# Kernel optimization log

Hardware: AMD Instinct MI355X
Metric: run time of the kernel (lower is better)

The kernel has to match this reference:

```python
import jax, jax.numpy as jnp
import numpy as np

B, T, E, D, A, V, EMB = 256, 64, 2048, 512, 512, 10000, 256

def _glorot(key, shape):
    lim = np.sqrt(6.0 / (shape[0] + shape[-1]))
    return jax.random.uniform(key, shape, jnp.float32, -lim, lim)

def setup_inputs() -> dict:
    key = jax.random.key(0)
    ks = jax.random.split(key, 16)
    return {
        'input_c': jax.random.randint(ks[0], (B, 1), 0, V),
        'hidden': jax.random.normal(ks[1], (B, D), jnp.float32),
        'carry': jax.random.normal(ks[2], (B, D), jnp.float32),
        'encoder_output': jax.random.normal(ks[3], (B, T, E), jnp.float32),
        'emb': jax.random.normal(ks[4], (V, EMB), jnp.float32) * 0.05,
        'w1': _glorot(ks[5], (D, A)),  'b1': jnp.zeros((A,), jnp.float32),
        'w2': _glorot(ks[6], (E, A)),  'b2': jnp.zeros((A,), jnp.float32),
        'v':  _glorot(ks[7], (A, 1)),  'bv': jnp.zeros((1,), jnp.float32),
        'wx': _glorot(ks[8], (E + EMB, 4 * D)),
        'wh': _glorot(ks[9], (D, 4 * D)),
        'bl': jnp.zeros((4 * D,), jnp.float32),
        'wp': _glorot(ks[10], (D, V)), 'bp': jnp.zeros((V,), jnp.float32),
    }

def reference(input_c, hidden, carry, encoder_output, emb, w1, b1, w2, b2, v, bv, wx, wh, bl, wp, bp):
    # embedding: [B,1] -> [B,EMB] after squeeze
    x = emb[input_c[:, 0]]
    # Bahdanau additive attention: score = v^T tanh(W1 h + W2 enc)
    q = hidden @ w1 + b1                                # [B,A]
    k = jnp.einsum('bte,ea->bta', encoder_output, w2) + b2  # [B,T,A]
    score = jnp.tanh(q[:, None, :] + k) @ v + bv        # [B,T,1]
    attn = jax.nn.softmax(score, axis=1)                # [B,T,1]
    context = jnp.sum(attn * encoder_output, axis=1)    # [B,E]
    # LSTM cell (keras gate order i,f,c,o); dropout inactive (training=False)
    lstm_in = jnp.concatenate([context, x], axis=-1)    # [B,E+EMB]
    z = lstm_in @ wx + hidden @ wh + bl                 # [B,4D]
    i, f, g, o = jnp.split(z, 4, axis=-1)
    c_new = jax.nn.sigmoid(f) * carry + jax.nn.sigmoid(i) * jnp.tanh(g)
    h_new = jax.nn.sigmoid(o) * jnp.tanh(c_new)
    logits = h_new @ wp + bp                            # [B,V]
    return logits, h_new, c_new
```

## Files before the change

### kernel.cpp

```cpp
#include <hip/hip_runtime.h>
#include <hip/hip_bf16.h>
#include <math.h>

#define BB 256
#define TT 64
#define EE 2048
#define DD 512
#define AA 512
#define VV 10000
#define VPAD 10240
#define EMBD 256
#define KLSTM (EE + EMBD + DD)
#define N4D (4 * DD)
#define MROWS (BB * TT)

using bf16x8 = __attribute__((ext_vector_type(8))) __bf16;
using f32x4  = __attribute__((ext_vector_type(4))) float;

#define GLL16(gp, lp) __builtin_amdgcn_global_load_lds( \
    (const __attribute__((address_space(1))) void*)(gp), \
    (__attribute__((address_space(3))) void*)(lp), 16, 0, 0)

__device__ __forceinline__ float sigf(float x) { return 1.f / (1.f + expf(-x)); }

__global__ void k_wt(const float* __restrict__ w2, const float* __restrict__ wx,
                     const float* __restrict__ wh, const float* __restrict__ wp,
                     __bf16* __restrict__ w2t, __bf16* __restrict__ wxh_t,
                     __bf16* __restrict__ wpt) {
    __shared__ float t[32][33];
    const int bid = blockIdx.x;
    const int tid = threadIdx.x;
    const int tx = tid & 31, ty = tid >> 5;

    if (bid < 1024) {
        const int k0 = (bid & 63) * 32, n0 = (bid >> 6) * 32;
        #pragma unroll
        for (int i = 0; i < 4; ++i)
            t[ty + 8 * i][tx] = w2[(size_t)(k0 + ty + 8 * i) * AA + n0 + tx];
        __syncthreads();
        #pragma unroll
        for (int i = 0; i < 4; ++i)
            w2t[(size_t)(n0 + ty + 8 * i) * EE + k0 + tx] = (__bf16)t[tx][ty + 8 * i];
    } else if (bid < 6656) {
        const int idx = bid - 1024;
        const int k0 = (idx % 88) * 32, n0 = (idx / 88) * 32;
        #pragma unroll
        for (int i = 0; i < 4; ++i) {
            int k = k0 + ty + 8 * i;
            const float* wrow = (k < EE + EMBD) ? &wx[(size_t)k * N4D]
                                                : &wh[(size_t)(k - EE - EMBD) * N4D];
            t[ty + 8 * i][tx] = wrow[n0 + tx];
        }
        __syncthreads();
        #pragma unroll
        for (int i = 0; i < 4; ++i)
            wxh_t[(size_t)(n0 + ty + 8 * i) * KLSTM + k0 + tx] = (__bf16)t[tx][ty + 8 * i];
    } else {
        const int idx = bid - 6656;
        const int k0 = (idx & 15) * 32, n0 = (idx >> 4) * 32;
        #pragma unroll
        for (int i = 0; i < 4; ++i) {
            int n = n0 + tx;
            t[ty + 8 * i][tx] = wp[(size_t)(k0 + ty + 8 * i) * VV + (n < VV ? n : VV - 1)];
        }
        __syncthreads();
        #pragma unroll
        for (int i = 0; i < 4; ++i)
            wpt[(size_t)(n0 + ty + 8 * i) * DD + k0 + tx] = (__bf16)t[tx][ty + 8 * i];
    }
}

__global__ void k_q(const float* __restrict__ hidden, const float* __restrict__ w1,
                    const float* __restrict__ b1, const float* __restrict__ b2,
                    float* __restrict__ qq) {
    __shared__ float hs[DD];
    const int b = blockIdx.x, tid = threadIdx.x;
    {
        float2 hv = *(const float2*)&hidden[(size_t)b * DD + 2 * tid];
        hs[2 * tid] = hv.x; hs[2 * tid + 1] = hv.y;
    }
    __syncthreads();
    const int a0 = 2 * tid;
    float2 acc = {0.f, 0.f};
    #pragma unroll 4
    for (int k = 0; k < DD; ++k) {
        float2 w = *(const float2*)&w1[(size_t)k * AA + a0];
        float h = hs[k];
        acc.x = fmaf(h, w.x, acc.x);
        acc.y = fmaf(h, w.y, acc.y);
    }
    qq[(size_t)b * AA + a0]     = acc.x + b1[a0]     + b2[a0];
    qq[(size_t)b * AA + a0 + 1] = acc.y + b1[a0 + 1] + b2[a0 + 1];
}

__global__ __launch_bounds__(1024, 8) void k_score(
        const float* __restrict__ enc, const __bf16* __restrict__ w2t,
        const float* __restrict__ qq, const float* __restrict__ vvec,
        float* __restrict__ spart) {
    __shared__ bf16x8 Abuf[128][8];
    __shared__ bf16x8 Bbuf[128][8];
    __shared__ float vsv[128];
    __shared__ float qsv2[2][128];
    __shared__ float wredL[16][32];
    const int tid = threadIdx.x;
    const int mb = blockIdx.x & 127, nb = blockIdx.x >> 7;
    const int m0 = mb * 128, n0 = nb * 128;
    const int l = tid & 63, wv = tid >> 6;
    const int wm = wv >> 2, wn = wv & 3;
    const int ar = l & 15, agr = l >> 4;

    if (tid < 256) {
        int i = tid >> 7, col = tid & 127;
        qsv2[i][col] = qq[(size_t)(2 * mb + i) * AA + n0 + col];
    } else if (tid < 384) {
        vsv[tid - 256] = vvec[n0 + tid - 256];
    }

    const int arow = tid >> 3, ag = tid & 7;
    const float* aptr = enc + (size_t)(m0 + arow) * EE + ag * 8;

    const int brow0 = wv * 8;
    const __bf16* bsrc = w2t + (size_t)(n0 + brow0 + (l >> 3)) * EE
                             + ((l & 7) ^ (l >> 3)) * 8;

    f32x4 acc[2][2];
    #pragma unroll
    for (int mi = 0; mi < 2; ++mi)
        #pragma unroll
        for (int ni = 0; ni < 2; ++ni)
            acc[mi][ni] = (f32x4){0.f, 0.f, 0.f, 0.f};

    const int NIT = EE / 64;
    for (int it = 0; it < NIT; ++it) {
        if (it > 0) __syncthreads();
        GLL16(bsrc + it * 64, &Bbuf[brow0][0]);
        {
            float4 u0 = *(const float4*)(aptr + it * 64);
            float4 u1 = *(const float4*)(aptr + it * 64 + 4);
            bf16x8 pk;
            pk[0] = (__bf16)u0.x; pk[1] = (__bf16)u0.y; pk[2] = (__bf16)u0.z; pk[3] = (__bf16)u0.w;
            pk[4] = (__bf16)u1.x; pk[5] = (__bf16)u1.y; pk[6] = (__bf16)u1.z; pk[7] = (__bf16)u1.w;
            Abuf[arow][ag ^ (arow & 7)] = pk;
        }
        __syncthreads();
        #pragma unroll
        for (int ks = 0; ks < 2; ++ks) {
            bf16x8 afr[2], bfr[2];
            #pragma unroll
            for (int mi = 0; mi < 2; ++mi)
                afr[mi] = Abuf[wm * 32 + mi * 16 + ar][(ks * 4 + agr) ^ (ar & 7)];
            #pragma unroll
            for (int ni = 0; ni < 2; ++ni)
                bfr[ni] = Bbuf[wn * 32 + ni * 16 + ar][(ks * 4 + agr) ^ (ar & 7)];
            #pragma unroll
            for (int mi = 0; mi < 2; ++mi)
                #pragma unroll
                for (int ni = 0; ni < 2; ++ni)
                    acc[mi][ni] = __builtin_amdgcn_mfma_f32_16x16x32_bf16(afr[mi], bfr[ni], acc[mi][ni], 0, 0, 0);
        }
    }

    float sred[2][4];
    #pragma unroll
    for (int mi = 0; mi < 2; ++mi)
        #pragma unroll
        for (int r = 0; r < 4; ++r) sred[mi][r] = 0.f;
    #pragma unroll
    for (int ni = 0; ni < 2; ++ni) {
        const int col = wn * 32 + ni * 16 + ar;
        const float va = vsv[col];
        const float qa = qsv2[wm >> 1][col];
        #pragma unroll
        for (int mi = 0; mi < 2; ++mi)
            #pragma unroll
            for (int r = 0; r < 4; ++r)
                sred[mi][r] += tanhf(qa + acc[mi][ni][r]) * va;
    }
    #pragma unroll
    for (int mi = 0; mi < 2; ++mi)
        #pragma unroll
        for (int r = 0; r < 4; ++r) {
            #pragma unroll
            for (int off = 1; off < 16; off <<= 1)
                sred[mi][r] += __shfl_xor(sred[mi][r], off, 64);
        }
    if (ar == 0) {
        #pragma unroll
        for (int mi = 0; mi < 2; ++mi)
            #pragma unroll
            for (int r = 0; r < 4; ++r)
                wredL[wv][mi * 16 + agr * 4 + r] = sred[mi][r];
    }
    __syncthreads();
    if (tid < 128) {
        const int wm4 = tid >> 5, rloc = tid & 31;
        float s = wredL[wm4 * 4 + 0][rloc] + wredL[wm4 * 4 + 1][rloc]
                + wredL[wm4 * 4 + 2][rloc] + wredL[wm4 * 4 + 3][rloc];
        spart[(size_t)nb * MROWS + m0 + tid] = s;
    }
}

__global__ void k_context(const float* __restrict__ enc, const float* __restrict__ spart,
                          const float* __restrict__ bv, float* __restrict__ ctx) {
    __shared__ float attn[TT];
    const int b = blockIdx.y;
    const int tid = threadIdx.x;
    if (tid < 64) {
        const int m = b * TT + tid;
        float s = spart[m] + spart[MROWS + m] + spart[2 * MROWS + m] + spart[3 * MROWS + m] + bv[0];
        float mx = s;
        #pragma unroll
        for (int off = 1; off < 64; off <<= 1) mx = fmaxf(mx, __shfl_xor(mx, off, 64));
        float p = expf(s - mx);
        float sum = p;
        #pragma unroll
        for (int off = 1; off < 64; off <<= 1) sum += __shfl_xor(sum, off, 64);
        attn[tid] = p / sum;
    }
    __syncthreads();
    const int e = blockIdx.x * 1024 + tid * 4;
    const float* encb = enc + (size_t)b * TT * EE + e;
    float4 acc = {0.f, 0.f, 0.f, 0.f};
    #pragma unroll 4
    for (int t = 0; t < TT; ++t) {
        float a = attn[t];
        float4 ev = *(const float4*)&encb[(size_t)t * EE];
        acc.x = fmaf(a, ev.x, acc.x);
        acc.y = fmaf(a, ev.y, acc.y);
        acc.z = fmaf(a, ev.z, acc.z);
        acc.w = fmaf(a, ev.w, acc.w);
    }
    *(float4*)&ctx[(size_t)b * EE + e] = acc;
}

#define ZKS 4
#define ZKC (KLSTM / ZKS)
#define ZNIT (ZKC / 32)
__global__ void k_z(const float* __restrict__ ctx, const float* __restrict__ emb,
                    const int* __restrict__ cidx, const float* __restrict__ hidden,
                    const __bf16* __restrict__ wt, float* __restrict__ zp) {
    __shared__ bf16x8 Abuf[32][ZKC / 8];
    __shared__ int cbs[32];
    const int tid = threadIdx.x;
    const int l = tid & 63, wv = tid >> 6;
    const int b0  = blockIdx.y * 32;
    const int kc0 = blockIdx.z * ZKC;
    const int nw  = blockIdx.x * 256 + wv * 64;

    if (tid < 32) cbs[tid] = cidx[b0 + tid];
    __syncthreads();

    {
        const int srow = tid >> 3, g0 = tid & 7;
        const int bg = b0 + srow;
        const int erow = cbs[srow];
        #pragma unroll
        for (int i = 0; i < 11; ++i) {
            int g = g0 + 8 * i;
            int k = kc0 + g * 8;
            const float* src;
            if (k < EE)             src = &ctx[(size_t)bg * EE + k];
            else if (k < EE + EMBD) src = &emb[(size_t)erow * EMBD + (k - EE)];
            else                    src = &hidden[(size_t)bg * DD + (k - EE - EMBD)];
            float4 u0 = *(const float4*)src;
            float4 u1 = *(const float4*)(src + 4);
            bf16x8 pk;
            pk[0] = (__bf16)u0.x; pk[1] = (__bf16)u0.y; pk[2] = (__bf16)u0.z; pk[3] = (__bf16)u0.w;
            pk[4] = (__bf16)u1.x; pk[5] = (__bf16)u1.y; pk[6] = (__bf16)u1.z; pk[7] = (__bf16)u1.w;
            Abuf[srow][g ^ (srow & 7)] = pk;
        }
    }
    __syncthreads();

    const int ar = l & 15, agr = l >> 4;
    const __bf16* bbase = wt + (size_t)(nw + ar) * KLSTM + kc0 + agr * 8;

    f32x4 acc[2][4];
    #pragma unroll
    for (int mt = 0; mt < 2; ++mt)
        #pragma unroll
        for (int f = 0; f < 4; ++f)
            acc[mt][f] = (f32x4){0.f, 0.f, 0.f, 0.f};

    bf16x8 bA[4], bBv[4];
    #pragma unroll
    for (int f = 0; f < 4; ++f)
        bA[f] = *(const bf16x8*)(bbase + (size_t)f * 16 * KLSTM);

    for (int itp = 0; itp < ZNIT / 2; ++itp) {
        const int it0 = 2 * itp, it1 = 2 * itp + 1;
        #pragma unroll
        for (int f = 0; f < 4; ++f)
            bBv[f] = *(const bf16x8*)(bbase + (size_t)f * 16 * KLSTM + it1 * 32);
        {
            bf16x8 a0 = Abuf[ar][(it0 * 4 + agr) ^ (ar & 7)];
            bf16x8 a1 = Abuf[16 + ar][(it0 * 4 + agr) ^ (ar & 7)];
            #pragma unroll
            for (int f = 0; f < 4; ++f) {
                acc[0][f] = __builtin_amdgcn_mfma_f32_16x16x32_bf16(a0, bA[f], acc[0][f], 0, 0, 0);
                acc[1][f] = __builtin_amdgcn_mfma_f32_16x16x32_bf16(a1, bA[f], acc[1][f], 0, 0, 0);
            }
        }
        const int it2 = (it1 + 1 < ZNIT) ? it1 + 1 : it1;
        #pragma unroll
        for (int f = 0; f < 4; ++f)
            bA[f] = *(const bf16x8*)(bbase + (size_t)f * 16 * KLSTM + it2 * 32);
        {
            bf16x8 a0 = Abuf[ar][(it1 * 4 + agr) ^ (ar & 7)];
            bf16x8 a1 = Abuf[16 + ar][(it1 * 4 + agr) ^ (ar & 7)];
            #pragma unroll
            for (int f = 0; f < 4; ++f) {
                acc[0][f] = __builtin_amdgcn_mfma_f32_16x16x32_bf16(a0, bBv[f], acc[0][f], 0, 0, 0);
                acc[1][f] = __builtin_amdgcn_mfma_f32_16x16x32_bf16(a1, bBv[f], acc[1][f], 0, 0, 0);
            }
        }
    }

    float* zpo = zp + (size_t)blockIdx.z * BB * N4D;
    #pragma unroll
    for (int mt = 0; mt < 2; ++mt)
        #pragma unroll
        for (int f = 0; f < 4; ++f)
            #pragma unroll
            for (int r = 0; r < 4; ++r)
                zpo[(size_t)(b0 + mt * 16 + agr * 4 + r) * N4D + nw + f * 16 + ar] = acc[mt][f][r];
}

__global__ void k_gates(const float* __restrict__ zp, const float* __restrict__ carry,
                        const float* __restrict__ bl,
                        float* __restrict__ hout, float* __restrict__ cout) {
    const int b = blockIdx.x, tid = threadIdx.x;
    const size_t P = (size_t)BB * N4D;
    #pragma unroll
    for (int r = 0; r < 2; ++r) {
        int d = tid + r * 256;
        float zi = bl[d], zf = bl[DD + d], zg = bl[2 * DD + d], zo = bl[3 * DD + d];
        #pragma unroll
        for (int ks = 0; ks < ZKS; ++ks) {
            const float* zb = zp + ks * P + (size_t)b * N4D;
            zi += zb[d];
            zf += zb[DD + d];
            zg += zb[2 * DD + d];
            zo += zb[3 * DD + d];
        }
        float c = carry[(size_t)b * DD + d];
        float cn = sigf(zf) * c + sigf(zi) * tanhf(zg);
        float hn = sigf(zo) * tanhf(cn);
        cout[(size_t)b * DD + d] = cn;
        hout[(size_t)b * DD + d] = hn;
    }
}

__global__ __launch_bounds__(256, 4) void k_logits(
        const float* __restrict__ hnew, const __bf16* __restrict__ wpt,
        const float* __restrict__ bp, float* __restrict__ logits) {
    __shared__ bf16x8 Abuf[64][8];
    __shared__ bf16x8 Bbuf[128][8];
    __shared__ float bps[128];
    const int tid = threadIdx.x;
    const int nb = blockIdx.x % 80, mb = blockIdx.x / 80;
    const int m0 = mb * 64, n0 = nb * 128;
    const int l = tid & 63, wv = tid >> 6;
    const int wm = wv >> 1, wn = wv & 1;
    const int ar = l & 15, agr = l >> 4;

    if (tid < 128) {
        int j = n0 + tid;
        bps[tid] = (j < VV) ? bp[j] : 0.f;
    }

    const int arow = tid >> 2, ag0 = (tid & 3) * 2;
    const float* aptr = hnew + (size_t)(m0 + arow) * DD + ag0 * 8;
    const int brow = tid >> 1, bg0 = (tid & 1) * 4;
    const __bf16* bptr = wpt + (size_t)(n0 + brow) * DD + bg0 * 8;

    f32x4 acc[2][4];
    #pragma unroll
    for (int mi = 0; mi < 2; ++mi)
        #pragma unroll
        for (int ni = 0; ni < 4; ++ni)
            acc[mi][ni] = (f32x4){0.f, 0.f, 0.f, 0.f};

    float4 af[4];
    bf16x8 bstg[4];
    #pragma unroll
    for (int j = 0; j < 4; ++j) af[j] = *(const float4*)(aptr + j * 4);
    #pragma unroll
    for (int i = 0; i < 4; ++i) bstg[i] = *(const bf16x8*)(bptr + i * 8);

    const int NIT = DD / 64;
    for (int it = 0; it < NIT; ++it) {
        if (it > 0) __syncthreads();
        {
            bf16x8 pk;
            pk[0] = (__bf16)af[0].x; pk[1] = (__bf16)af[0].y; pk[2] = (__bf16)af[0].z; pk[3] = (__bf16)af[0].w;
            pk[4] = (__bf16)af[1].x; pk[5] = (__bf16)af[1].y; pk[6] = (__bf16)af[1].z; pk[7] = (__bf16)af[1].w;
            Abuf[arow][ag0 ^ (arow & 7)] = pk;
            pk[0] = (__bf16)af[2].x; pk[1] = (__bf16)af[2].y; pk[2] = (__bf16)af[2].z; pk[3] = (__bf16)af[2].w;
            pk[4] = (__bf16)af[3].x; pk[5] = (__bf16)af[3].y; pk[6] = (__bf16)af[3].z; pk[7] = (__bf16)af[3].w;
            Abuf[arow][(ag0 + 1) ^ (arow & 7)] = pk;
        }
        #pragma unroll
        for (int i = 0; i < 4; ++i)
            Bbuf[brow][(bg0 + i) ^ (brow & 7)] = bstg[i];
        if (it + 1 < NIT) {
            const int k1 = (it + 1) * 64;
            #pragma unroll
            for (int j = 0; j < 4; ++j) af[j] = *(const float4*)(aptr + k1 + j * 4);
            #pragma unroll
            for (int i = 0; i < 4; ++i) bstg[i] = *(const bf16x8*)(bptr + k1 + i * 8);
        }
        __syncthreads();
        #pragma unroll
        for (int ks = 0; ks < 2; ++ks) {
            bf16x8 afr[2], bfr[4];
            #pragma unroll
            for (int mi = 0; mi < 2; ++mi)
                afr[mi] = Abuf[wm * 32 + mi * 16 + ar][(ks * 4 + agr) ^ (ar & 7)];
            #pragma unroll
            for (int ni = 0; ni < 4; ++ni)
                bfr[ni] = Bbuf[wn * 64 + ni * 16 + ar][(ks * 4 + agr) ^ (ar & 7)];
            #pragma unroll
            for (int mi = 0; mi < 2; ++mi)
                #pragma unroll
                for (int ni = 0; ni < 4; ++ni)
                    acc[mi][ni] = __builtin_amdgcn_mfma_f32_16x16x32_bf16(afr[mi], bfr[ni], acc[mi][ni], 0, 0, 0);
        }
    }

    #pragma unroll
    for (int mi = 0; mi < 2; ++mi)
        #pragma unroll
        for (int ni = 0; ni < 4; ++ni) {
            const int colL = wn * 64 + ni * 16 + ar;
            const int col = n0 + colL;
            if (col < VV) {
                const float bb = bps[colL];
                #pragma unroll
                for (int r = 0; r < 4; ++r) {
                    const int row = m0 + wm * 32 + mi * 16 + agr * 4 + r;
                    logits[(size_t)row * VV + col] = acc[mi][ni][r] + bb;
                }
            }
        }
}

extern "C" void kernel_launch(void* const* d_in, const int* in_sizes, int n_in,
                              void* d_out, int out_size, void* d_ws, size_t ws_size,
                              hipStream_t stream) {
    const int*   cidx   = (const int*)d_in[0];
    const float* hidden = (const float*)d_in[1];
    const float* carry  = (const float*)d_in[2];
    const float* enc    = (const float*)d_in[3];
    const float* emb    = (const float*)d_in[4];
    const float* w1     = (const float*)d_in[5];
    const float* b1     = (const float*)d_in[6];
    const float* w2     = (const float*)d_in[7];
    const float* b2     = (const float*)d_in[8];
    const float* vvec   = (const float*)d_in[9];
    const float* bv     = (const float*)d_in[10];
    const float* wx     = (const float*)d_in[11];
    const float* wh     = (const float*)d_in[12];
    const float* bl     = (const float*)d_in[13];
    const float* wp     = (const float*)d_in[14];
    const float* bp     = (const float*)d_in[15];

    float* out    = (float*)d_out;
    float* logits = out;
    float* hout   = out + (size_t)BB * VV;
    float* cout   = hout + (size_t)BB * DD;

    float* ws    = (float*)d_ws;
    float* qq    = ws;
    float* score = qq + (size_t)BB * AA;
    float* ctx   = score + (size_t)BB * TT;
    float* zp    = ctx + (size_t)BB * EE;
    __bf16* wxh_t = (__bf16*)(zp + (size_t)ZKS * BB * N4D);
    float* spart = (float*)(wxh_t + (size_t)N4D * KLSTM);
    __bf16* wpt  = (__bf16*)(spart + (size_t)4 * MROWS);
    __bf16* w2t  = (__bf16*)ctx;

    hipLaunchKernelGGL(k_wt,      dim3(11776),               dim3(256), 0, stream,
                       w2, wx, wh, wp, w2t, wxh_t, wpt);
    hipLaunchKernelGGL(k_q,       dim3(BB),                  dim3(256), 0, stream, hidden, w1, b1, b2, qq);
    hipLaunchKernelGGL(k_score,   dim3(512),                 dim3(1024), 0, stream, enc, w2t, qq, vvec, spart);
    hipLaunchKernelGGL(k_context, dim3(2, BB),               dim3(256), 0, stream, enc, spart, bv, ctx);
    hipLaunchKernelGGL(k_z,       dim3(N4D / 256, BB / 32, ZKS), dim3(256), 0, stream, ctx, emb, cidx, hidden, wxh_t, zp);
    hipLaunchKernelGGL(k_gates,   dim3(BB),                  dim3(256), 0, stream, zp, carry, bl, hout, cout);
    hipLaunchKernelGGL(k_logits,  dim3(320),                 dim3(256), 0, stream, hout, wpt, bp, logits);
}
```

Measured before the change: 167.0 us.

## Double-buffer LDS tiles in attention score GEMM to overlap loads with MFMA

Splits the A and B shared-memory tiles in the score kernel into two buffers. The next K-slice is prefetched (global-to-LDS for B, register loads for A) while MFMAs run on the current slice, and each iteration ends with one barrier instead of two. This aims to hide global memory latency behind compute. In exchange it doubles LDS use for the tiles, which may lower occupancy for the 1024-thread blocks, and raises register pressure from holding the prefetched A values.

```diff
diff --git a/kernel.cpp b/kernel.cpp
--- a/kernel.cpp
+++ b/kernel.cpp
@@ -97,8 +97,8 @@
         const float* __restrict__ enc, const __bf16* __restrict__ w2t,
         const float* __restrict__ qq, const float* __restrict__ vvec,
         float* __restrict__ spart) {
-    __shared__ bf16x8 Abuf[128][8];
-    __shared__ bf16x8 Bbuf[128][8];
+    __shared__ bf16x8 Abuf[2][128][8];
+    __shared__ bf16x8 Bbuf[2][128][8];
     __shared__ float vsv[128];
     __shared__ float qsv2[2][128];
     __shared__ float wredL[16][32];
@@ -118,6 +118,7 @@
 
     const int arow = tid >> 3, ag = tid & 7;
     const float* aptr = enc + (size_t)(m0 + arow) * EE + ag * 8;
+    const int asw = ag ^ (arow & 7);
 
     const int brow0 = wv * 8;
     const __bf16* bsrc = w2t + (size_t)(n0 + brow0 + (l >> 3)) * EE
@@ -130,34 +131,50 @@
         for (int ni = 0; ni < 2; ++ni)
             acc[mi][ni] = (f32x4){0.f, 0.f, 0.f, 0.f};
 
+    GLL16(bsrc, &Bbuf[0][brow0][0]);
+    {
+        float4 u0 = *(const float4*)(aptr);
+        float4 u1 = *(const float4*)(aptr + 4);
+        bf16x8 pk;
+        pk[0] = (__bf16)u0.x; pk[1] = (__bf16)u0.y; pk[2] = (__bf16)u0.z; pk[3] = (__bf16)u0.w;
+        pk[4] = (__bf16)u1.x; pk[5] = (__bf16)u1.y; pk[6] = (__bf16)u1.z; pk[7] = (__bf16)u1.w;
+        Abuf[0][arow][asw] = pk;
+    }
+    __syncthreads();
+
     const int NIT = EE / 64;
     for (int it = 0; it < NIT; ++it) {
-        if (it > 0) __syncthreads();
-        GLL16(bsrc + it * 64, &Bbuf[brow0][0]);
-        {
-            float4 u0 = *(const float4*)(aptr + it * 64);
-            float4 u1 = *(const float4*)(aptr + it * 64 + 4);
-            bf16x8 pk;
-            pk[0] = (__bf16)u0.x; pk[1] = (__bf16)u0.y; pk[2] = (__bf16)u0.z; pk[3] = (__bf16)u0.w;
-            pk[4] = (__bf16)u1.x; pk[5] = (__bf16)u1.y; pk[6] = (__bf16)u1.z; pk[7] = (__bf16)u1.w;
-            Abuf[arow][ag ^ (arow & 7)] = pk;
-        }
-        __syncthreads();
+        const int cur = it & 1;
+        const bool more = (it + 1 < NIT);
+        float4 u0, u1;
+        if (more) {
+            const int k1 = (it + 1) * 64;
+            GLL16(bsrc + k1, &Bbuf[cur ^ 1][brow0][0]);
+            u0 = *(const float4*)(aptr + k1);
+            u1 = *(const float4*)(aptr + k1 + 4);
+        }
         #pragma unroll
         for (int ks = 0; ks < 2; ++ks) {
             bf16x8 afr[2], bfr[2];
             #pragma unroll
             for (int mi = 0; mi < 2; ++mi)
-                afr[mi] = Abuf[wm * 32 + mi * 16 + ar][(ks * 4 + agr) ^ (ar & 7)];
+                afr[mi] = Abuf[cur][wm * 32 + mi * 16 + ar][(ks * 4 + agr) ^ (ar & 7)];
             #pragma unroll
             for (int ni = 0; ni < 2; ++ni)
-                bfr[ni] = Bbuf[wn * 32 + ni * 16 + ar][(ks * 4 + agr) ^ (ar & 7)];
+                bfr[ni] = Bbuf[cur][wn * 32 + ni * 16 + ar][(ks * 4 + agr) ^ (ar & 7)];
             #pragma unroll
             for (int mi = 0; mi < 2; ++mi)
                 #pragma unroll
                 for (int ni = 0; ni < 2; ++ni)
                     acc[mi][ni] = __builtin_amdgcn_mfma_f32_16x16x32_bf16(afr[mi], bfr[ni], acc[mi][ni], 0, 0, 0);
         }
+        if (more) {
+            bf16x8 pk;
+            pk[0] = (__bf16)u0.x; pk[1] = (__bf16)u0.y; pk[2] = (__bf16)u0.z; pk[3] = (__bf16)u0.w;
+            pk[4] = (__bf16)u1.x; pk[5] = (__bf16)u1.y; pk[6] = (__bf16)u1.z; pk[7] = (__bf16)u1.w;
+            Abuf[cur ^ 1][arow][asw] = pk;
+        }
+        __syncthreads();
     }
 
     float sred[2][4];
```

Result: slower. 175.3 us (+5.0%).
